# Performance work log

Measured on AMD Instinct MI355X. Metric: run time of the kernel, lower is better.

## Reference

```python
import jax, jax.numpy as jnp
import numpy as np

H = 4096; NH = 32; HD = 128; SCALE = HD ** -0.5
PREFILLS = [1024, 512, 768, 256]; DOFF = sum(PREFILLS)
DEC = 32; LMAX = 512; T = DOFF + DEC
NLORA = 4; RANK = 16
SEG = [0, 648, 1296, 1944, 2592]  # static lora segment offsets (cumsum of lens)
NEG = -1e30


def _rope_tables(pos):
    # pos: int array [...]; returns cos/sin of shape [..., HD]
    inv = 1.0 / (10000.0 ** (jnp.arange(0, HD, 2, dtype=jnp.float32) / HD))
    freqs = pos.astype(jnp.float32)[..., None] * inv
    emb = jnp.concatenate([freqs, freqs], axis=-1)
    return jnp.cos(emb), jnp.sin(emb)


def _apply_rope(x, cos, sin):
    # x: [..., HD]; cos/sin broadcastable to x
    x1, x2 = x[..., :HD // 2], x[..., HD // 2:]
    return x * cos + jnp.concatenate([-x2, x1], axis=-1) * sin


def _add_lora(y, x, wa, wb):
    # Punica add_lora: per-segment y += (x @ wa[i]) @ wb[i], segments static
    for i in range(NLORA):
        s, e = SEG[i], SEG[i + 1]
        y = y.at[s:e].add((x[s:e] @ wa[i]) @ wb[i])
    return y


def setup_inputs() -> dict:
    key = jax.random.key(0)
    ks = jax.random.split(key, 16)
    sc = np.float32(1.0 / np.sqrt(H))
    lsc = np.float32(1.0 / np.sqrt(H))
    inp = {
        "hidden_states": jax.random.normal(ks[0], (T, H), jnp.float32),
        "wq": jax.random.normal(ks[1], (H, H), jnp.float32) * sc,
        "wk": jax.random.normal(ks[2], (H, H), jnp.float32) * sc,
        "wv": jax.random.normal(ks[3], (H, H), jnp.float32) * sc,
        "wo": jax.random.normal(ks[4], (H, H), jnp.float32) * sc,
        "la_q": jax.random.normal(ks[5], (NLORA, H, RANK), jnp.float32) * lsc,
        "lb_q": jax.random.normal(ks[6], (NLORA, RANK, H), jnp.float32) * lsc,
        "la_k": jax.random.normal(ks[7], (NLORA, H, RANK), jnp.float32) * lsc,
        "lb_k": jax.random.normal(ks[8], (NLORA, RANK, H), jnp.float32) * lsc,
        "la_v": jax.random.normal(ks[9], (NLORA, H, RANK), jnp.float32) * lsc,
        "lb_v": jax.random.normal(ks[10], (NLORA, RANK, H), jnp.float32) * lsc,
        "la_o": jax.random.normal(ks[11], (NLORA, H, RANK), jnp.float32) * lsc,
        "lb_o": jax.random.normal(ks[12], (NLORA, RANK, H), jnp.float32) * lsc,
        "k_cache": jax.random.normal(ks[13], (DEC, LMAX, NH, HD), jnp.float32),
        "v_cache": jax.random.normal(ks[14], (DEC, LMAX, NH, HD), jnp.float32),
        "kv_lens": jax.random.randint(ks[15], (DEC,), 0, 450, jnp.int32),
    }
    return inp


def reference(hidden_states, wq, wk, wv, wo, la_q, lb_q, la_k, lb_k,
              la_v, lb_v, la_o, lb_o, k_cache, v_cache, kv_lens):
    # fused QKV + segmented batched LoRA
    q = _add_lora(hidden_states @ wq, hidden_states, la_q, lb_q)
    k = _add_lora(hidden_states @ wk, hidden_states, la_k, lb_k)
    v = _add_lora(hidden_states @ wv, hidden_states, la_v, lb_v)

    outs = []
    # ragged prefill: per-request causal attention with inline rotary (beg=0)
    off = 0
    for s_len in PREFILLS:
        qi = q[off:off + s_len].reshape(s_len, NH, HD)
        ki = k[off:off + s_len].reshape(s_len, NH, HD)
        vi = v[off:off + s_len].reshape(s_len, NH, HD)
        cos, sin = _rope_tables(jnp.arange(s_len))
        cos, sin = cos[:, None, :], sin[:, None, :]
        qi = _apply_rope(qi, cos, sin)
        ki = _apply_rope(ki, cos, sin)
        scores = jnp.einsum('qhd,khd->hqk', qi, ki) * SCALE
        causal = jnp.tril(jnp.ones((s_len, s_len), bool))
        scores = jnp.where(causal[None], scores, NEG)
        p = jax.nn.softmax(scores, axis=-1)
        outs.append(jnp.einsum('hqk,khd->qhd', p, vi).reshape(s_len, H))
        off += s_len

    # paged/batched decode: append new k/v at kv_lens, rope-on-the-fly attention
    qd = q[DOFF:].reshape(DEC, NH, HD)
    kd = k[DOFF:].reshape(DEC, NH, HD)
    vd = v[DOFF:].reshape(DEC, NH, HD)
    b = jnp.arange(DEC)
    kc = k_cache.at[b, kv_lens].set(kd)
    vc = v_cache.at[b, kv_lens].set(vd)
    cosq, sinq = _rope_tables(kv_lens)            # new token position = kv_len
    qd = _apply_rope(qd, cosq[:, None, :], sinq[:, None, :])
    cosk, sink = _rope_tables(jnp.arange(LMAX))   # cache positions 0..LMAX-1
    kc_r = _apply_rope(kc, cosk[None, :, None, :], sink[None, :, None, :])
    scores = jnp.einsum('bhd,blhd->bhl', qd, kc_r) * SCALE
    valid = jnp.arange(LMAX)[None, :] <= kv_lens[:, None]  # [DEC, LMAX]
    scores = jnp.where(valid[:, None, :], scores, NEG)
    p = jax.nn.softmax(scores, axis=-1)
    outs.append(jnp.einsum('bhl,blhd->bhd', p, vc).reshape(DEC, H))

    attn = jnp.concatenate(outs, axis=0)          # [T, H]
    o = attn @ wo
    o = _add_lora(o, attn, la_o, lb_o)
    return o
```

## Files before the change

kernel.cpp:

```cpp
#include <hip/hip_runtime.h>
#include <hip/hip_bf16.h>


#define H_    4096
#define NH_   32
#define HD_   128
#define T_    2592
#define DOFF_ 2560
#define DEC_  32
#define LMAX_ 512
#define RANK_ 16
#define MPAD_ 2816

__constant__ float SCALE_ = 0.08838834764831845f;

typedef __bf16 bf16x8 __attribute__((ext_vector_type(8)));
typedef __bf16 bf16x4 __attribute__((ext_vector_type(4)));
typedef float  f32x4  __attribute__((ext_vector_type(4)));

__device__ __forceinline__ void async_cp16(const __bf16* g, __bf16* l) {
    __builtin_amdgcn_global_load_lds(
        (const __attribute__((address_space(1))) void*)g,
        (__attribute__((address_space(3))) void*)l, 16, 0, 0);
}

__global__ __launch_bounds__(256)
void convert_bf16_kernel(const float* __restrict__ src, __bf16* __restrict__ dst, int n8)
{
    const int stride = gridDim.x * blockDim.x;
    for (int i = blockIdx.x * blockDim.x + threadIdx.x; i < n8; i += stride) {
        float4 a = ((const float4*)src)[i * 2];
        float4 b = ((const float4*)src)[i * 2 + 1];
        bf16x8 w;
        w[0] = (__bf16)a.x; w[1] = (__bf16)a.y; w[2] = (__bf16)a.z; w[3] = (__bf16)a.w;
        w[4] = (__bf16)b.x; w[5] = (__bf16)b.y; w[6] = (__bf16)b.z; w[7] = (__bf16)b.w;
        ((bf16x8*)dst)[i] = w;
    }
}

__global__ __launch_bounds__(256)
void transpose_bf16_kernel(const float* __restrict__ W0, const float* __restrict__ W1,
                           const float* __restrict__ W2,
                           __bf16* __restrict__ T0, __bf16* __restrict__ T1, __bf16* __restrict__ T2)
{
    const float* W = (blockIdx.z == 0) ? W0 : (blockIdx.z == 1 ? W1 : W2);
    __bf16* To     = (blockIdx.z == 0) ? T0 : (blockIdx.z == 1 ? T1 : T2);
    __shared__ float s[32][33];
    const int bx = blockIdx.x * 32;
    const int by = blockIdx.y * 32;
    const int r  = threadIdx.x >> 3;
    const int c4 = (threadIdx.x & 7) * 4;
    float4 v = *(const float4*)&W[(size_t)(by + r) * H_ + bx + c4];
    s[r][c4] = v.x; s[r][c4 + 1] = v.y; s[r][c4 + 2] = v.z; s[r][c4 + 3] = v.w;
    __syncthreads();
    bf16x4 o;
    o[0] = (__bf16)s[c4 + 0][r]; o[1] = (__bf16)s[c4 + 1][r];
    o[2] = (__bf16)s[c4 + 2][r]; o[3] = (__bf16)s[c4 + 3][r];
    *(bf16x4*)&To[(size_t)(bx + r) * H_ + by + c4] = o;
}

__global__ __launch_bounds__(256)
void lora_tmp_kernel(const float* __restrict__ X,
                     const float* __restrict__ la0, const float* __restrict__ la1,
                     const float* __restrict__ la2, __bf16* __restrict__ TMP16)
{
    const int r = blockIdx.x;
    const int si = (r < 648) ? 0 : (r < 1296 ? 1 : (r < 1944 ? 2 : 3));
    const int c    = threadIdx.x & 15;
    const int part = threadIdx.x >> 4;
    const float* xr = X + (size_t)r * H_;
    const float* wa0 = la0 + (size_t)si * H_ * RANK_;
    const float* wa1 = la1 + (size_t)si * H_ * RANK_;
    const float* wa2 = la2 + (size_t)si * H_ * RANK_;
    float s0 = 0.f, s1 = 0.f, s2 = 0.f;
    const int h0 = part * 256;
    for (int h = h0; h < h0 + 256; ++h) {
        const float xv = xr[h];
        s0 += xv * wa0[(size_t)h * RANK_ + c];
        s1 += xv * wa1[(size_t)h * RANK_ + c];
        s2 += xv * wa2[(size_t)h * RANK_ + c];
    }
    __shared__ float red[3][16][17];
    red[0][part][c] = s0; red[1][part][c] = s1; red[2][part][c] = s2;
    __syncthreads();
    if (threadIdx.x < 192) {
        const int z = threadIdx.x >> 6, cc = threadIdx.x & 63;
        float t = 0.f;
        if ((cc >> 4) == si) {
            #pragma unroll
            for (int p = 0; p < 16; ++p) t += red[z][p][cc & 15];
        }
        TMP16[((size_t)z * MPAD_ + r) * 64 + cc] = (__bf16)t;
    }
}

__global__ __launch_bounds__(256)
void lora_tmp_bf16_kernel(const __bf16* __restrict__ X,
                          const float* __restrict__ la, __bf16* __restrict__ TMPo16)
{
    const int r = blockIdx.x;
    const int si = (r < 648) ? 0 : (r < 1296 ? 1 : (r < 1944 ? 2 : 3));
    const float* wa = la + (size_t)si * H_ * RANK_;
    const int c    = threadIdx.x & 15;
    const int part = threadIdx.x >> 4;
    const __bf16* xr = X + (size_t)r * H_;
    float s = 0.f;
    const int h0 = part * 256;
    for (int h = h0; h < h0 + 256; ++h) s += (float)xr[h] * wa[(size_t)h * RANK_ + c];
    __shared__ float red[16][17];
    red[part][c] = s;
    __syncthreads();
    if (threadIdx.x < 64) {
        const int cc = threadIdx.x;
        float t = 0.f;
        if ((cc >> 4) == si) {
            #pragma unroll
            for (int p = 0; p < 16; ++p) t += red[p][cc & 15];
        }
        TMPo16[(size_t)r * 64 + cc] = (__bf16)t;
    }
}

__global__ __launch_bounds__(256)
void wb_build_kernel(const float* __restrict__ lbq, const float* __restrict__ lbk,
                     const float* __restrict__ lbv, const float* __restrict__ lbo,
                     __bf16* __restrict__ WB16, __bf16* __restrict__ WBo16)
{
    const int z = blockIdx.x;
    const int n = blockIdx.y * 256 + threadIdx.x;
    const float* lb = (z == 0) ? lbq : (z == 1 ? lbk : (z == 2 ? lbv : lbo));
    __bf16* dst = (z < 3) ? WB16 + ((size_t)z * H_ + n) * 64 : WBo16 + (size_t)n * 64;
    __bf16 row[64];
    #pragma unroll
    for (int si = 0; si < 4; ++si)
        #pragma unroll
        for (int c = 0; c < 16; ++c)
            row[si * 16 + c] = (__bf16)lb[((size_t)si * 16 + c) * H_ + n];
    #pragma unroll
    for (int i = 0; i < 8; ++i) *(bf16x8*)&dst[i * 8] = *(const bf16x8*)&row[i * 8];
}

__global__ __launch_bounds__(512, 2)
void gemm_qkv(const __bf16* __restrict__ A, const __bf16* __restrict__ Bt,
              const __bf16* __restrict__ TMP16, const __bf16* __restrict__ WB16,
              __bf16* __restrict__ O0, __bf16* __restrict__ O1, __bf16* __restrict__ O2, int M)
{
    const int hw = blockIdx.y * 21 + blockIdx.x;
    const int work = (hw & 7) * 126 + (hw >> 3);
    const int bm0 = (work % 21) * 128;
    const int bn0 = (work / 21) * 256;

    __shared__ __align__(16) __bf16 Asl[3][128 * 64];
    __shared__ __align__(16) __bf16 Bsl[3][256 * 64];

    const int tid = threadIdx.x, lane = tid & 63, wid = tid >> 6;
    const int wr = wid >> 2, wc = wid & 3;
    const int fr = lane & 15, fq = lane >> 4;

    int arow[2], aoff[2], brow[4], boff[4];
    #pragma unroll
    for (int i = 0; i < 2; ++i) {
        const int ci = i * 512 + tid;
        arow[i] = ci >> 3;
        aoff[i] = ((ci & 7) ^ (arow[i] & 7)) * 8;
    }
    #pragma unroll
    for (int i = 0; i < 4; ++i) {
        const int ci = i * 512 + tid;
        brow[i] = ci >> 3;
        boff[i] = ((ci & 7) ^ (brow[i] & 7)) * 8;
    }
    const __bf16* Ab = A  + (size_t)bm0 * H_;
    const __bf16* Bb = Bt + (size_t)bn0 * H_;

    auto stageA = [&](int buf, int kt2) {
        const int kb = kt2 * 64;
        #pragma unroll
        for (int i = 0; i < 2; ++i)
            async_cp16(Ab + (size_t)arow[i] * H_ + kb + aoff[i],
                       &Asl[buf][(i * 512 + wid * 64) * 8]);
    };
    auto stageB1 = [&](int buf, int kt2) {
        async_cp16(Bb + (size_t)brow[0] * H_ + kt2 * 64 + boff[0],
                   &Bsl[buf][(wid * 64) * 8]);
    };
    auto stageB3 = [&](int buf, int kt2) {
        const int kb = kt2 * 64;
        #pragma unroll
        for (int i = 1; i < 4; ++i)
            async_cp16(Bb + (size_t)brow[i] * H_ + kb + boff[i],
                       &Bsl[buf][(i * 512 + wid * 64) * 8]);
    };
    auto rdA = [&](int buf, int kh, int mi) -> bf16x8 {
        const int row = wr * 64 + mi * 16 + fr;
        const int pc  = (kh * 4 + fq) ^ (row & 7);
        return *(const bf16x8*)&Asl[buf][row * 64 + pc * 8];
    };
    auto rdB = [&](int buf, int kh, int nj) -> bf16x8 {
        const int row = wc * 64 + nj * 16 + fr;
        const int pc  = (kh * 4 + fq) ^ (row & 7);
        return *(const bf16x8*)&Bsl[buf][row * 64 + pc * 8];
    };

    f32x4 acc[4][4] = {};

    stageA(0, 0); stageB1(0, 0); stageB3(0, 0);
    stageA(1, 1); stageB1(1, 1); stageB3(1, 1);
    asm volatile("s_waitcnt vmcnt(6)");
    __builtin_amdgcn_sched_barrier(0);
    __builtin_amdgcn_s_barrier();

    const int NT = H_ / 64;
    int cur = 0, nxt = 2;
    for (int kt = 0; kt < NT; ++kt) {
        const bool pf = (kt + 2 < NT);
        bf16x8 af[4], bfr[4];

        #pragma unroll
        for (int mi = 0; mi < 4; ++mi) af[mi] = rdA(cur, 0, mi);
        #pragma unroll
        for (int nj = 0; nj < 4; ++nj) bfr[nj] = rdB(cur, 0, nj);
        if (pf) { stageA(nxt, kt + 2); stageB1(nxt, kt + 2); }
        __builtin_amdgcn_s_barrier();
        asm volatile("s_waitcnt lgkmcnt(0)");
        __builtin_amdgcn_sched_barrier(0);
        __builtin_amdgcn_s_setprio(1);
        #pragma unroll
        for (int mi = 0; mi < 4; ++mi)
            #pragma unroll
            for (int nj = 0; nj < 4; ++nj)
                acc[mi][nj] = __builtin_amdgcn_mfma_f32_16x16x32_bf16(af[mi], bfr[nj], acc[mi][nj], 0, 0, 0);
        __builtin_amdgcn_s_setprio(0);
        __builtin_amdgcn_s_barrier();

        #pragma unroll
        for (int mi = 0; mi < 4; ++mi) af[mi] = rdA(cur, 1, mi);
        #pragma unroll
        for (int nj = 0; nj < 4; ++nj) bfr[nj] = rdB(cur, 1, nj);
        if (pf) stageB3(nxt, kt + 2);
        __builtin_amdgcn_s_barrier();
        asm volatile("s_waitcnt lgkmcnt(0)");
        __builtin_amdgcn_sched_barrier(0);
        __builtin_amdgcn_s_setprio(1);
        #pragma unroll
        for (int mi = 0; mi < 4; ++mi)
            #pragma unroll
            for (int nj = 0; nj < 4; ++nj)
                acc[mi][nj] = __builtin_amdgcn_mfma_f32_16x16x32_bf16(af[mi], bfr[nj], acc[mi][nj], 0, 0, 0);
        __builtin_amdgcn_s_setprio(0);
        if (pf)               asm volatile("s_waitcnt vmcnt(6)");
        else if (kt + 1 < NT) asm volatile("s_waitcnt vmcnt(0)");
        __builtin_amdgcn_sched_barrier(0);
        __builtin_amdgcn_s_barrier();

        cur = (cur == 2) ? 0 : cur + 1;
        nxt = (nxt == 2) ? 0 : nxt + 1;
    }

    const int colbase = bn0 + wc * 64;
    const int mat = colbase >> 12;
    __bf16* O = (mat == 0) ? O0 : (mat == 1 ? O1 : O2);
    const __bf16* TPm = TMP16 + (size_t)mat * MPAD_ * 64;
    bf16x8 aT[4][2], bW[4][2];
    #pragma unroll
    for (int mi = 0; mi < 4; ++mi)
        #pragma unroll
        for (int kh = 0; kh < 2; ++kh)
            aT[mi][kh] = *(const bf16x8*)&TPm[(size_t)(bm0 + wr * 64 + mi * 16 + fr) * 64 + kh * 32 + fq * 8];
    #pragma unroll
    for (int nj = 0; nj < 4; ++nj)
        #pragma unroll
        for (int kh = 0; kh < 2; ++kh)
            bW[nj][kh] = *(const bf16x8*)&WB16[(size_t)(colbase + nj * 16 + fr) * 64 + kh * 32 + fq * 8];
    #pragma unroll
    for (int mi = 0; mi < 4; ++mi)
        #pragma unroll
        for (int nj = 0; nj < 4; ++nj) {
            acc[mi][nj] = __builtin_amdgcn_mfma_f32_16x16x32_bf16(aT[mi][0], bW[nj][0], acc[mi][nj], 0, 0, 0);
            acc[mi][nj] = __builtin_amdgcn_mfma_f32_16x16x32_bf16(aT[mi][1], bW[nj][1], acc[mi][nj], 0, 0, 0);
        }
    #pragma unroll
    for (int mi = 0; mi < 4; ++mi)
        #pragma unroll
        for (int nj = 0; nj < 4; ++nj) {
            const int cc = (colbase + nj * 16 + fr) & 4095;
            #pragma unroll
            for (int rr = 0; rr < 4; ++rr) {
                const int row = bm0 + wr * 64 + mi * 16 + fq * 4 + rr;
                if (row < M) O[(size_t)row * H_ + cc] = (__bf16)acc[mi][nj][rr];
            }
        }
}

__global__ __launch_bounds__(512, 2)
void gemm_out(const __bf16* __restrict__ A, const __bf16* __restrict__ Bt,
              const __bf16* __restrict__ TMPo16, const __bf16* __restrict__ WBo16,
              float* __restrict__ C, int M, int Ntot)
{
    const int NY = gridDim.y;
    const int total = gridDim.x * NY;
    const int bid = blockIdx.x * NY + blockIdx.y;
    const int q = total >> 3, r8 = total & 7;
    const int xcd = bid & 7, j = bid >> 3;
    const int swz = (xcd < r8 ? xcd * (q + 1) : r8 * (q + 1) + (xcd - r8) * q) + j;
    const int bm0 = (swz / NY) * 256;
    const int bn0 = (swz % NY) * 192;

    __shared__ __align__(16) __bf16 Asl[2][256 * 64];
    __shared__ __align__(16) __bf16 Bsl[2][192 * 64];

    const int tid = threadIdx.x, lane = tid & 63, wid = tid >> 6;
    const int wr = wid >> 2, wc = wid & 3;
    const int fr = lane & 15, fq = lane >> 4;

    int arow[4], aoff[4], brow[3], boff[3];
    #pragma unroll
    for (int i = 0; i < 4; ++i) {
        const int ci = i * 512 + tid;
        arow[i] = ci >> 3;
        aoff[i] = ((ci & 7) ^ (arow[i] & 7)) * 8;
    }
    #pragma unroll
    for (int i = 0; i < 3; ++i) {
        const int ci = i * 512 + tid;
        brow[i] = ci >> 3;
        boff[i] = ((ci & 7) ^ (brow[i] & 7)) * 8;
    }
    const __bf16* Ab = A  + (size_t)bm0 * H_;
    const __bf16* Bb = Bt + (size_t)bn0 * H_;

    auto stage = [&](int buf, int kt1) {
        const int kb = kt1 * 64;
        #pragma unroll
        for (int i = 0; i < 4; ++i)
            async_cp16(Ab + (size_t)arow[i] * H_ + kb + aoff[i],
                       &Asl[buf][(i * 512 + wid * 64) * 8]);
        #pragma unroll
        for (int i = 0; i < 3; ++i)
            async_cp16(Bb + (size_t)brow[i] * H_ + kb + boff[i],
                       &Bsl[buf][(i * 512 + wid * 64) * 8]);
    };
    auto rdA = [&](int buf, int kh, int mi) -> bf16x8 {
        const int row = wr * 128 + mi * 16 + fr;
        const int kc  = kh * 4 + fq;
        return *(const bf16x8*)&Asl[buf][row * 64 + ((kc ^ (row & 7)) << 3)];
    };
    auto rdB = [&](int buf, int kh, int nj) -> bf16x8 {
        const int row = wc * 48 + nj * 16 + fr;
        const int kc  = kh * 4 + fq;
        return *(const bf16x8*)&Bsl[buf][row * 64 + ((kc ^ (row & 7)) << 3)];
    };

    f32x4 acc[8][3] = {};

    stage(0, 0);
    asm volatile("s_waitcnt vmcnt(0)");
    __builtin_amdgcn_sched_barrier(0);
    __builtin_amdgcn_s_barrier();

    const int NT = H_ / 64;
    for (int kt = 0; kt < NT; ++kt) {
        const int cur = kt & 1, nb = cur ^ 1;
        const bool pf = (kt + 1 < NT);
        bf16x8 af[8], bfr[3];

        #pragma unroll
        for (int mi = 0; mi < 8; ++mi) af[mi] = rdA(cur, 0, mi);
        #pragma unroll
        for (int nj = 0; nj < 3; ++nj) bfr[nj] = rdB(cur, 0, nj);
        if (pf) stage(nb, kt + 1);
        __builtin_amdgcn_s_barrier();
        asm volatile("s_waitcnt lgkmcnt(0)");
        __builtin_amdgcn_sched_barrier(0);
        __builtin_amdgcn_s_setprio(1);
        #pragma unroll
        for (int mi = 0; mi < 8; ++mi)
            #pragma unroll
            for (int nj = 0; nj < 3; ++nj)
                acc[mi][nj] = __builtin_amdgcn_mfma_f32_16x16x32_bf16(af[mi], bfr[nj], acc[mi][nj], 0, 0, 0);
        __builtin_amdgcn_s_setprio(0);
        __builtin_amdgcn_s_barrier();

        #pragma unroll
        for (int mi = 0; mi < 8; ++mi) af[mi] = rdA(cur, 1, mi);
        #pragma unroll
        for (int nj = 0; nj < 3; ++nj) bfr[nj] = rdB(cur, 1, nj);
        __builtin_amdgcn_s_barrier();
        asm volatile("s_waitcnt lgkmcnt(0)");
        __builtin_amdgcn_sched_barrier(0);
        __builtin_amdgcn_s_setprio(1);
        #pragma unroll
        for (int mi = 0; mi < 8; ++mi)
            #pragma unroll
            for (int nj = 0; nj < 3; ++nj)
                acc[mi][nj] = __builtin_amdgcn_mfma_f32_16x16x32_bf16(af[mi], bfr[nj], acc[mi][nj], 0, 0, 0);
        __builtin_amdgcn_s_setprio(0);
        asm volatile("s_waitcnt vmcnt(0)");
        __builtin_amdgcn_sched_barrier(0);
        __builtin_amdgcn_s_barrier();
    }

    const int colw = bn0 + wc * 48;
    bf16x8 aT[8][2], bW[3][2];
    #pragma unroll
    for (int mi = 0; mi < 8; ++mi)
        #pragma unroll
        for (int kh = 0; kh < 2; ++kh)
            aT[mi][kh] = *(const bf16x8*)&TMPo16[(size_t)(bm0 + wr * 128 + mi * 16 + fr) * 64 + kh * 32 + fq * 8];
    #pragma unroll
    for (int nj = 0; nj < 3; ++nj)
        #pragma unroll
        for (int kh = 0; kh < 2; ++kh)
            bW[nj][kh] = *(const bf16x8*)&WBo16[(size_t)(colw + nj * 16 + fr) * 64 + kh * 32 + fq * 8];
    #pragma unroll
    for (int mi = 0; mi < 8; ++mi)
        #pragma unroll
        for (int nj = 0; nj < 3; ++nj) {
            acc[mi][nj] = __builtin_amdgcn_mfma_f32_16x16x32_bf16(aT[mi][0], bW[nj][0], acc[mi][nj], 0, 0, 0);
            acc[mi][nj] = __builtin_amdgcn_mfma_f32_16x16x32_bf16(aT[mi][1], bW[nj][1], acc[mi][nj], 0, 0, 0);
        }
    #pragma unroll
    for (int mi = 0; mi < 8; ++mi)
        #pragma unroll
        for (int nj = 0; nj < 3; ++nj) {
            const int col = colw + nj * 16 + fr;
            if (col < Ntot) {
                #pragma unroll
                for (int rr = 0; rr < 4; ++rr) {
                    const int row = bm0 + wr * 128 + mi * 16 + fq * 4 + rr;
                    if (row < M) C[(size_t)row * H_ + col] = acc[mi][nj][rr];
                }
            }
        }
}

__global__ void rope_table_kernel(float* __restrict__ cost, float* __restrict__ sint)
{
    const int p = blockIdx.x;
    const int i = threadIdx.x;
    const float inv = powf(10000.f, -(float)(2 * i) / (float)HD_);
    const float a = (float)p * inv;
    cost[p * 64 + i] = cosf(a);
    sint[p * 64 + i] = sinf(a);
}

__global__ __launch_bounds__(256)
void rope16_kernel(__bf16* __restrict__ q16, __bf16* __restrict__ k16,
                   const int* __restrict__ kv_lens,
                   const float* __restrict__ cost, const float* __restrict__ sint)
{
    const int r = blockIdx.x;
    int pos; bool dok;
    if (r < DOFF_) {
        if      (r < 1024) pos = r;
        else if (r < 1536) pos = r - 1024;
        else if (r < 2304) pos = r - 1536;
        else               pos = r - 2304;
        dok = true;
    } else {
        pos = kv_lens[r - DOFF_];
        dok = false;
    }
    const int tid = threadIdx.x;
    const int h = tid >> 3, sub = tid & 7;
    const int i0 = sub * 8;
    const size_t b1 = (size_t)r * H_ + h * HD_ + i0;
    const size_t b2 = b1 + 64;

    float cs[8], sn[8];
    #pragma unroll
    for (int j = 0; j < 8; ++j) { cs[j] = cost[pos * 64 + i0 + j]; sn[j] = sint[pos * 64 + i0 + j]; }

    {
        bf16x8 x1 = *(const bf16x8*)&q16[b1], x2 = *(const bf16x8*)&q16[b2];
        bf16x8 o1, o2;
        #pragma unroll
        for (int j = 0; j < 8; ++j) {
            const float f1 = (float)x1[j], f2 = (float)x2[j];
            o1[j] = (__bf16)(f1 * cs[j] - f2 * sn[j]);
            o2[j] = (__bf16)(f2 * cs[j] + f1 * sn[j]);
        }
        *(bf16x8*)&q16[b1] = o1; *(bf16x8*)&q16[b2] = o2;
    }
    if (dok) {
        bf16x8 x1 = *(const bf16x8*)&k16[b1], x2 = *(const bf16x8*)&k16[b2];
        bf16x8 o1, o2;
        #pragma unroll
        for (int j = 0; j < 8; ++j) {
            const float f1 = (float)x1[j], f2 = (float)x2[j];
            o1[j] = (__bf16)(f1 * cs[j] - f2 * sn[j]);
            o2[j] = (__bf16)(f2 * cs[j] + f1 * sn[j]);
        }
        *(bf16x8*)&k16[b1] = o1; *(bf16x8*)&k16[b2] = o2;
    }
}

__global__ __launch_bounds__(256)
void transpose_v_kernel(const __bf16* __restrict__ v16, __bf16* __restrict__ vT)
{
    __shared__ __bf16 s[64][136];
    const int tb = blockIdx.x;
    const int h  = blockIdx.y;
    const int tid = threadIdx.x;
    #pragma unroll
    for (int i = 0; i < 4; ++i) {
        const int idx = i * 256 + tid;
        const int row = idx >> 4;
        const int c8  = (idx & 15) * 8;
        *(bf16x8*)&s[row][c8] = *(const bf16x8*)&v16[(size_t)(tb * 64 + row) * H_ + h * HD_ + c8];
    }
    __syncthreads();
    #pragma unroll
    for (int i = 0; i < 4; ++i) {
        const int idx = i * 256 + tid;
        const int d = idx >> 3;
        const int c = idx & 7;
        bf16x8 w;
        #pragma unroll
        for (int j = 0; j < 8; ++j) w[j] = s[c * 8 + j][d];
        *(bf16x8*)&vT[(size_t)(h * HD_ + d) * T_ + tb * 64 + c * 8] = w;
    }
}

__global__ __launch_bounds__(256)
void prefill_attn_mfma(const __bf16* __restrict__ q16, const __bf16* __restrict__ k16,
                       const __bf16* __restrict__ vT, __bf16* __restrict__ attn16)
{
    const int qb = blockIdx.x;
    int soff, qoff;
    if      (qb < 16) { soff = 0;    qoff = qb * 64; }
    else if (qb < 24) { soff = 1024; qoff = (qb - 16) * 64; }
    else if (qb < 36) { soff = 1536; qoff = (qb - 24) * 64; }
    else              { soff = 2304; qoff = (qb - 36) * 64; }
    const int h = blockIdx.y;

    __shared__ __align__(16) __bf16 Kl[64 * 128];
    __shared__ __align__(16) __bf16 Vl[128 * 64];
    __shared__ __align__(16) __bf16 Pl[4][16 * 64];

    const int tid = threadIdx.x, lane = tid & 63, wid = tid >> 6;
    const int fr = lane & 15, fq = lane >> 4;

    const int grow0 = soff + qoff + wid * 16;
    bf16x8 qf[4];
    #pragma unroll
    for (int ks = 0; ks < 4; ++ks)
        qf[ks] = *(const bf16x8*)&q16[(size_t)(grow0 + fr) * H_ + h * HD_ + ks * 32 + fq * 8];

    float m[4], l[4];
    #pragma unroll
    for (int r = 0; r < 4; ++r) { m[r] = -1e30f; l[r] = 0.f; }
    f32x4 o[8] = {};

    const int ntiles = qoff / 64 + 1;
    for (int t = 0; t < ntiles; ++t) {
        const int kt = t * 64;
        #pragma unroll
        for (int i = 0; i < 4; ++i) {
            const int chunk = i * 256 + tid;
            const int row = chunk >> 4, c = chunk & 15;
            async_cp16(k16 + (size_t)(soff + kt + row) * H_ + h * HD_ + ((c ^ (row & 7)) * 8),
                       Kl + (size_t)(i * 256 + wid * 64) * 8);
        }
        #pragma unroll
        for (int i = 0; i < 4; ++i) {
            const int chunk = i * 256 + tid;
            const int row = chunk >> 3, c = chunk & 7;
            async_cp16(vT + (size_t)(h * HD_ + row) * T_ + soff + kt + ((c ^ (row & 7)) * 8),
                       Vl + (size_t)(i * 256 + wid * 64) * 8);
        }
        __syncthreads();

        f32x4 s[4] = {};
        #pragma unroll
        for (int sub = 0; sub < 4; ++sub)
            #pragma unroll
            for (int ks = 0; ks < 4; ++ks) {
                bf16x8 b = *(const bf16x8*)&Kl[(sub * 16 + fr) * 128 + (((ks * 4 + fq) ^ (fr & 7)) * 8)];
                s[sub] = __builtin_amdgcn_mfma_f32_16x16x32_bf16(qf[ks], b, s[sub], 0, 0, 0);
            }

        float p[4][4];
        #pragma unroll
        for (int sub = 0; sub < 4; ++sub)
            #pragma unroll
            for (int r = 0; r < 4; ++r) {
                const int qpos = qoff + wid * 16 + fq * 4 + r;
                const int kpos = kt + sub * 16 + fr;
                p[sub][r] = (kpos <= qpos) ? s[sub][r] * SCALE_ : -1e30f;
            }
        float fsc[4];
        #pragma unroll
        for (int r = 0; r < 4; ++r) {
            float tm = fmaxf(fmaxf(p[0][r], p[1][r]), fmaxf(p[2][r], p[3][r]));
            tm = fmaxf(tm, __shfl_xor(tm, 1));
            tm = fmaxf(tm, __shfl_xor(tm, 2));
            tm = fmaxf(tm, __shfl_xor(tm, 4));
            tm = fmaxf(tm, __shfl_xor(tm, 8));
            const float mn = fmaxf(m[r], tm);
            fsc[r] = __expf(m[r] - mn);
            m[r] = mn;
            float ls = 0.f;
            #pragma unroll
            for (int sub = 0; sub < 4; ++sub) {
                p[sub][r] = __expf(p[sub][r] - mn);
                ls += p[sub][r];
            }
            l[r] = l[r] * fsc[r] + ls;
        }
        #pragma unroll
        for (int c = 0; c < 8; ++c)
            #pragma unroll
            for (int r = 0; r < 4; ++r) o[c][r] *= fsc[r];

        #pragma unroll
        for (int sub = 0; sub < 4; ++sub)
            #pragma unroll
            for (int r = 0; r < 4; ++r) {
                const int qr = fq * 4 + r;
                Pl[wid][qr * 64 + ((sub * 16 + fr) ^ ((qr & 7) << 3))] = (__bf16)p[sub][r];
            }
        bf16x8 pa[2];
        #pragma unroll
        for (int a = 0; a < 2; ++a)
            pa[a] = *(const bf16x8*)&Pl[wid][fr * 64 + (((a * 4 + fq) ^ (fr & 7)) * 8)];

        #pragma unroll
        for (int a = 0; a < 2; ++a)
            #pragma unroll
            for (int c = 0; c < 8; ++c) {
                bf16x8 bv = *(const bf16x8*)&Vl[(c * 16 + fr) * 64 + (((a * 4 + fq) ^ (fr & 7)) * 8)];
                o[c] = __builtin_amdgcn_mfma_f32_16x16x32_bf16(pa[a], bv, o[c], 0, 0, 0);
            }
        __syncthreads();
    }

    float inv[4];
    #pragma unroll
    for (int r = 0; r < 4; ++r) {
        float ls = l[r];
        ls += __shfl_xor(ls, 1); ls += __shfl_xor(ls, 2);
        ls += __shfl_xor(ls, 4); ls += __shfl_xor(ls, 8);
        inv[r] = 1.f / ls;
    }
    #pragma unroll
    for (int c = 0; c < 8; ++c)
        #pragma unroll
        for (int r = 0; r < 4; ++r)
            attn16[(size_t)(grow0 + fq * 4 + r) * H_ + h * HD_ + c * 16 + fr] = (__bf16)(o[c][r] * inv[r]);
}

__global__ __launch_bounds__(256)
void decode_attn_kernel(const __bf16* __restrict__ q16, const __bf16* __restrict__ k16,
                        const __bf16* __restrict__ v16, const float* __restrict__ kc,
                        const float* __restrict__ vc, const int* __restrict__ kv_lens,
                        const float* __restrict__ cost, const float* __restrict__ sint,
                        __bf16* __restrict__ attn16)
{
    const int b = blockIdx.x, h = blockIdx.y;
    const int kvlen = kv_lens[b];
    const int L = kvlen + 1;
    const int tid = threadIdx.x, lane = tid & 63, w = tid >> 6;

    __shared__ float sc_s[LMAX_];
    __shared__ float red[4];
    __shared__ float oacc[HD_];

    const __bf16* qrow = q16 + (size_t)(DOFF_ + b) * H_ + h * HD_;
    const float q1 = (float)qrow[lane], q2 = (float)qrow[lane + 64];
    const __bf16* kdrow = k16 + (size_t)(DOFF_ + b) * H_ + h * HD_;

    for (int l = w; l < L; l += 4) {
        float k1, k2;
        if (l == kvlen) { k1 = (float)kdrow[lane]; k2 = (float)kdrow[lane + 64]; }
        else {
            const float* src = kc + (((size_t)b * LMAX_ + l) * NH_ + h) * HD_;
            k1 = src[lane]; k2 = src[lane + 64];
        }
        const float c = cost[l * 64 + lane], s = sint[l * 64 + lane];
        float d = q1 * (k1 * c - k2 * s) + q2 * (k2 * c + k1 * s);
        #pragma unroll
        for (int off = 1; off < 64; off <<= 1) d += __shfl_xor(d, off);
        if (lane == 0) sc_s[l] = d * SCALE_;
    }
    __syncthreads();

    float mx = -1e30f;
    for (int i = tid; i < L; i += 256) mx = fmaxf(mx, sc_s[i]);
    #pragma unroll
    for (int off = 1; off < 64; off <<= 1) mx = fmaxf(mx, __shfl_xor(mx, off));
    if (lane == 0) red[w] = mx;
    __syncthreads();
    mx = fmaxf(fmaxf(red[0], red[1]), fmaxf(red[2], red[3]));
    __syncthreads();

    float sum = 0.f;
    for (int i = tid; i < L; i += 256) { const float e = __expf(sc_s[i] - mx); sc_s[i] = e; sum += e; }
    #pragma unroll
    for (int off = 1; off < 64; off <<= 1) sum += __shfl_xor(sum, off);
    if (lane == 0) red[w] = sum;
    __syncthreads();
    sum = red[0] + red[1] + red[2] + red[3];
    const float inv = 1.f / sum;

    const int d = tid & 127, team = tid >> 7;
    const __bf16* vdrow = v16 + (size_t)(DOFF_ + b) * H_ + h * HD_;
    float acc = 0.f;
    for (int l = team; l < L; l += 2) {
        float vv;
        if (l == kvlen) vv = (float)vdrow[d];
        else            vv = vc[(((size_t)b * LMAX_ + l) * NH_ + h) * HD_ + d];
        acc += sc_s[l] * vv;
    }
    if (team == 1) oacc[d] = acc;
    __syncthreads();
    if (team == 0) attn16[(size_t)(DOFF_ + b) * H_ + h * HD_ + d] = (__bf16)((acc + oacc[d]) * inv);
}

extern "C" void kernel_launch(void* const* d_in, const int* in_sizes, int n_in,
                              void* d_out, int out_size, void* d_ws, size_t ws_size,
                              hipStream_t stream)
{
    const float* hs     = (const float*)d_in[0];
    const float* wq     = (const float*)d_in[1];
    const float* wk     = (const float*)d_in[2];
    const float* wv     = (const float*)d_in[3];
    const float* wo     = (const float*)d_in[4];
    const float* la_q   = (const float*)d_in[5];
    const float* lb_q   = (const float*)d_in[6];
    const float* la_k   = (const float*)d_in[7];
    const float* lb_k   = (const float*)d_in[8];
    const float* la_v   = (const float*)d_in[9];
    const float* lb_v   = (const float*)d_in[10];
    const float* la_o   = (const float*)d_in[11];
    const float* lb_o   = (const float*)d_in[12];
    const float* kcache = (const float*)d_in[13];
    const float* vcache = (const float*)d_in[14];
    const int*   kvlen  = (const int*)d_in[15];
    float* out = (float*)d_out;

    float*  costab = (float*)d_ws;
    float*  sintab = costab + 1024 * 64;
    __bf16* TMP16  = (__bf16*)(sintab + 1024 * 64);
    __bf16* TMPo16 = TMP16 + (size_t)3 * MPAD_ * 64;
    __bf16* WB16   = TMPo16 + (size_t)MPAD_ * 64;
    __bf16* WBo16  = WB16 + (size_t)3 * H_ * 64;
    __bf16* q16    = WBo16 + (size_t)4352 * 64;
    __bf16* k16    = q16 + (size_t)T_ * H_;
    __bf16* v16    = k16 + (size_t)T_ * H_;
    __bf16* hsb    = v16 + (size_t)T_ * H_;
    __bf16* wT     = hsb + (size_t)MPAD_ * H_;
    __bf16* vT     = wT + (size_t)H_ * H_;
    __bf16* attn16 = hsb;

    const int N8 = T_ * H_ / 8;

    rope_table_kernel<<<dim3(1024), dim3(64), 0, stream>>>(costab, sintab);
    convert_bf16_kernel<<<dim3(2048), dim3(256), 0, stream>>>(hs, hsb, N8);
    transpose_bf16_kernel<<<dim3(128, 128, 3), dim3(256), 0, stream>>>(
        wq, wk, wv, wT, wT + (size_t)H_ * H_, wT + (size_t)2 * H_ * H_);
    lora_tmp_kernel<<<dim3(T_), dim3(256), 0, stream>>>(hs, la_q, la_k, la_v, TMP16);
    wb_build_kernel<<<dim3(4, 16), dim3(256), 0, stream>>>(lb_q, lb_k, lb_v, lb_o, WB16, WBo16);
    gemm_qkv<<<dim3(21, 48), dim3(512), 0, stream>>>(
        hsb, wT, TMP16, WB16, q16, k16, v16, T_);
    rope16_kernel<<<dim3(T_), dim3(256), 0, stream>>>(q16, k16, kvlen, costab, sintab);
    transpose_v_kernel<<<dim3(40, 32), dim3(256), 0, stream>>>(v16, vT);
    prefill_attn_mfma<<<dim3(40, 32), dim3(256), 0, stream>>>(q16, k16, vT, attn16);
    decode_attn_kernel<<<dim3(DEC_, NH_), dim3(256), 0, stream>>>(q16, k16, v16, kcache, vcache,
                                                                  kvlen, costab, sintab, attn16);
    transpose_bf16_kernel<<<dim3(128, 128, 1), dim3(256), 0, stream>>>(wo, wo, wo, wT, wT, wT);
    lora_tmp_bf16_kernel<<<dim3(T_), dim3(256), 0, stream>>>(attn16, la_o, TMPo16);
    gemm_out<<<dim3(11, 22), dim3(512), 0, stream>>>(
        attn16, wT, TMPo16, WBo16, out, T_, H_);
}
```

Baseline: 971.5 us.

## Double-buffer prefill attention, lazy rescale, fuse hs convert with LoRA, bigger transpose tiles

Prefill attention now keeps two K/V LDS buffers and prefetches tile t+2 while computing tile t, using explicit vmcnt waits and raw barriers. It also skips the online-softmax rescale unless the running max grows by more than a threshold, and raises wave priority around the MFMA blocks. Separately, the hidden-state bf16 conversion is folded into the LoRA-A kernel, and the weight transpose moves to 64x64 tiles with 16-byte stores. The double buffering doubles LDS use, which may lower occupancy, and the lazy rescale relies on exp staying bounded when the max is stale.

After: 942.0 us. -3.0%, faster.

```diff
diff --git a/kernel.cpp b/kernel.cpp
--- a/kernel.cpp
+++ b/kernel.cpp
@@ -25,50 +25,24 @@
 }
 
 __global__ __launch_bounds__(256)
-void convert_bf16_kernel(const float* __restrict__ src, __bf16* __restrict__ dst, int n8)
-{
-    const int stride = gridDim.x * blockDim.x;
-    for (int i = blockIdx.x * blockDim.x + threadIdx.x; i < n8; i += stride) {
-        float4 a = ((const float4*)src)[i * 2];
-        float4 b = ((const float4*)src)[i * 2 + 1];
-        bf16x8 w;
-        w[0] = (__bf16)a.x; w[1] = (__bf16)a.y; w[2] = (__bf16)a.z; w[3] = (__bf16)a.w;
-        w[4] = (__bf16)b.x; w[5] = (__bf16)b.y; w[6] = (__bf16)b.z; w[7] = (__bf16)b.w;
-        ((bf16x8*)dst)[i] = w;
-    }
-}
-
-__global__ __launch_bounds__(256)
-void transpose_bf16_kernel(const float* __restrict__ W0, const float* __restrict__ W1,
-                           const float* __restrict__ W2,
-                           __bf16* __restrict__ T0, __bf16* __restrict__ T1, __bf16* __restrict__ T2)
-{
-    const float* W = (blockIdx.z == 0) ? W0 : (blockIdx.z == 1 ? W1 : W2);
-    __bf16* To     = (blockIdx.z == 0) ? T0 : (blockIdx.z == 1 ? T1 : T2);
-    __shared__ float s[32][33];
-    const int bx = blockIdx.x * 32;
-    const int by = blockIdx.y * 32;
-    const int r  = threadIdx.x >> 3;
-    const int c4 = (threadIdx.x & 7) * 4;
-    float4 v = *(const float4*)&W[(size_t)(by + r) * H_ + bx + c4];
-    s[r][c4] = v.x; s[r][c4 + 1] = v.y; s[r][c4 + 2] = v.z; s[r][c4 + 3] = v.w;
-    __syncthreads();
-    bf16x4 o;
-    o[0] = (__bf16)s[c4 + 0][r]; o[1] = (__bf16)s[c4 + 1][r];
-    o[2] = (__bf16)s[c4 + 2][r]; o[3] = (__bf16)s[c4 + 3][r];
-    *(bf16x4*)&To[(size_t)(bx + r) * H_ + by + c4] = o;
-}
-
-__global__ __launch_bounds__(256)
-void lora_tmp_kernel(const float* __restrict__ X,
-                     const float* __restrict__ la0, const float* __restrict__ la1,
-                     const float* __restrict__ la2, __bf16* __restrict__ TMP16)
+void hs_prep_kernel(const float* __restrict__ X, __bf16* __restrict__ Xb,
+                    const float* __restrict__ la0, const float* __restrict__ la1,
+                    const float* __restrict__ la2, __bf16* __restrict__ TMP16)
 {
     const int r = blockIdx.x;
+    const int tid = threadIdx.x;
+    const float* xr = X + (size_t)r * H_;
+    __bf16* br = Xb + (size_t)r * H_;
+    #pragma unroll
+    for (int i = 0; i < 4; ++i) {
+        float4 v = ((const float4*)xr)[tid + i * 256];
+        bf16x4 w; w[0] = (__bf16)v.x; w[1] = (__bf16)v.y; w[2] = (__bf16)v.z; w[3] = (__bf16)v.w;
+        ((bf16x4*)br)[tid + i * 256] = w;
+    }
+
     const int si = (r < 648) ? 0 : (r < 1296 ? 1 : (r < 1944 ? 2 : 3));
-    const int c    = threadIdx.x & 15;
-    const int part = threadIdx.x >> 4;
-    const float* xr = X + (size_t)r * H_;
+    const int c    = tid & 15;
+    const int part = tid >> 4;
     const float* wa0 = la0 + (size_t)si * H_ * RANK_;
     const float* wa1 = la1 + (size_t)si * H_ * RANK_;
     const float* wa2 = la2 + (size_t)si * H_ * RANK_;
@@ -83,14 +57,46 @@
     __shared__ float red[3][16][17];
     red[0][part][c] = s0; red[1][part][c] = s1; red[2][part][c] = s2;
     __syncthreads();
-    if (threadIdx.x < 192) {
-        const int z = threadIdx.x >> 6, cc = threadIdx.x & 63;
+    if (tid < 192) {
+        const int z = tid >> 6, cc = tid & 63;
         float t = 0.f;
         if ((cc >> 4) == si) {
             #pragma unroll
             for (int p = 0; p < 16; ++p) t += red[z][p][cc & 15];
         }
         TMP16[((size_t)z * MPAD_ + r) * 64 + cc] = (__bf16)t;
+    }
+}
+
+__global__ __launch_bounds__(256)
+void transpose_bf16_kernel(const float* __restrict__ W0, const float* __restrict__ W1,
+                           const float* __restrict__ W2,
+                           __bf16* __restrict__ T0, __bf16* __restrict__ T1, __bf16* __restrict__ T2)
+{
+    const float* W = (blockIdx.z == 0) ? W0 : (blockIdx.z == 1 ? W1 : W2);
+    __bf16* To     = (blockIdx.z == 0) ? T0 : (blockIdx.z == 1 ? T1 : T2);
+    __shared__ float s[64][65];
+    const int bx = blockIdx.x * 64;
+    const int by = blockIdx.y * 64;
+    const int tid = threadIdx.x;
+    #pragma unroll
+    for (int i = 0; i < 4; ++i) {
+        const int idx = i * 256 + tid;
+        const int r  = idx >> 4;
+        const int c4 = (idx & 15) * 4;
+        float4 v = *(const float4*)&W[(size_t)(by + r) * H_ + bx + c4];
+        s[r][c4] = v.x; s[r][c4 + 1] = v.y; s[r][c4 + 2] = v.z; s[r][c4 + 3] = v.w;
+    }
+    __syncthreads();
+    #pragma unroll
+    for (int i = 0; i < 2; ++i) {
+        const int idx = i * 256 + tid;
+        const int n  = idx >> 3;
+        const int kc = (idx & 7) * 8;
+        bf16x8 w;
+        #pragma unroll
+        for (int j = 0; j < 8; ++j) w[j] = (__bf16)s[kc + j][n];
+        *(bf16x8*)&To[(size_t)(bx + n) * H_ + by + kc] = w;
     }
 }
 
@@ -534,8 +540,8 @@
     else              { soff = 2304; qoff = (qb - 36) * 64; }
     const int h = blockIdx.y;
 
-    __shared__ __align__(16) __bf16 Kl[64 * 128];
-    __shared__ __align__(16) __bf16 Vl[128 * 64];
+    __shared__ __align__(16) __bf16 Kl[2][64 * 128];
+    __shared__ __align__(16) __bf16 Vl[2][128 * 64];
     __shared__ __align__(16) __bf16 Pl[4][16 * 64];
 
     const int tid = threadIdx.x, lane = tid & 63, wid = tid >> 6;
@@ -547,38 +553,57 @@
     for (int ks = 0; ks < 4; ++ks)
         qf[ks] = *(const bf16x8*)&q16[(size_t)(grow0 + fr) * H_ + h * HD_ + ks * 32 + fq * 8];
 
-    float m[4], l[4];
-    #pragma unroll
-    for (int r = 0; r < 4; ++r) { m[r] = -1e30f; l[r] = 0.f; }
-    f32x4 o[8] = {};
-
-    const int ntiles = qoff / 64 + 1;
-    for (int t = 0; t < ntiles; ++t) {
+    auto stageK = [&](int buf, int t) {
         const int kt = t * 64;
         #pragma unroll
         for (int i = 0; i < 4; ++i) {
             const int chunk = i * 256 + tid;
             const int row = chunk >> 4, c = chunk & 15;
             async_cp16(k16 + (size_t)(soff + kt + row) * H_ + h * HD_ + ((c ^ (row & 7)) * 8),
-                       Kl + (size_t)(i * 256 + wid * 64) * 8);
-        }
+                       Kl[buf] + (size_t)(i * 256 + wid * 64) * 8);
+        }
+    };
+    auto stageV = [&](int buf, int t) {
+        const int kt = t * 64;
         #pragma unroll
         for (int i = 0; i < 4; ++i) {
             const int chunk = i * 256 + tid;
             const int row = chunk >> 3, c = chunk & 7;
             async_cp16(vT + (size_t)(h * HD_ + row) * T_ + soff + kt + ((c ^ (row & 7)) * 8),
-                       Vl + (size_t)(i * 256 + wid * 64) * 8);
-        }
-        __syncthreads();
+                       Vl[buf] + (size_t)(i * 256 + wid * 64) * 8);
+        }
+    };
+
+    float m[4], l[4];
+    #pragma unroll
+    for (int r = 0; r < 4; ++r) { m[r] = -1e30f; l[r] = 0.f; }
+    f32x4 o[8] = {};
+
+    const int ntiles = qoff / 64 + 1;
+    stageK(0, 0); stageV(0, 0);
+    if (ntiles > 1) {
+        stageK(1, 1); stageV(1, 1);
+        asm volatile("s_waitcnt vmcnt(8)");
+    } else {
+        asm volatile("s_waitcnt vmcnt(0)");
+    }
+    __builtin_amdgcn_sched_barrier(0);
+    __builtin_amdgcn_s_barrier();
+
+    for (int t = 0; t < ntiles; ++t) {
+        const int b = t & 1;
+        const int kt = t * 64;
 
         f32x4 s[4] = {};
+        __builtin_amdgcn_s_setprio(1);
         #pragma unroll
         for (int sub = 0; sub < 4; ++sub)
             #pragma unroll
             for (int ks = 0; ks < 4; ++ks) {
-                bf16x8 b = *(const bf16x8*)&Kl[(sub * 16 + fr) * 128 + (((ks * 4 + fq) ^ (fr & 7)) * 8)];
-                s[sub] = __builtin_amdgcn_mfma_f32_16x16x32_bf16(qf[ks], b, s[sub], 0, 0, 0);
+                bf16x8 bk = *(const bf16x8*)&Kl[b][(sub * 16 + fr) * 128 + (((ks * 4 + fq) ^ (fr & 7)) * 8)];
+                s[sub] = __builtin_amdgcn_mfma_f32_16x16x32_bf16(qf[ks], bk, s[sub], 0, 0, 0);
             }
+        __builtin_amdgcn_s_setprio(0);
 
         float p[4][4];
         #pragma unroll
@@ -589,7 +614,7 @@
                 const int kpos = kt + sub * 16 + fr;
                 p[sub][r] = (kpos <= qpos) ? s[sub][r] * SCALE_ : -1e30f;
             }
-        float fsc[4];
+        float tm2[4];
         #pragma unroll
         for (int r = 0; r < 4; ++r) {
             float tm = fmaxf(fmaxf(p[0][r], p[1][r]), fmaxf(p[2][r], p[3][r]));
@@ -597,21 +622,32 @@
             tm = fmaxf(tm, __shfl_xor(tm, 2));
             tm = fmaxf(tm, __shfl_xor(tm, 4));
             tm = fmaxf(tm, __shfl_xor(tm, 8));
-            const float mn = fmaxf(m[r], tm);
-            fsc[r] = __expf(m[r] - mn);
-            m[r] = mn;
+            tm2[r] = tm;
+        }
+        bool need = false;
+        #pragma unroll
+        for (int r = 0; r < 4; ++r) need |= (tm2[r] > m[r] + 8.f);
+        if (__any(need)) {
+            #pragma unroll
+            for (int r = 0; r < 4; ++r) {
+                const float mn = fmaxf(m[r], tm2[r]);
+                const float f  = __expf(m[r] - mn);
+                m[r] = mn;
+                l[r] *= f;
+                #pragma unroll
+                for (int c = 0; c < 8; ++c) o[c][r] *= f;
+            }
+        }
+        #pragma unroll
+        for (int r = 0; r < 4; ++r) {
             float ls = 0.f;
             #pragma unroll
             for (int sub = 0; sub < 4; ++sub) {
-                p[sub][r] = __expf(p[sub][r] - mn);
+                p[sub][r] = __expf(p[sub][r] - m[r]);
                 ls += p[sub][r];
             }
-            l[r] = l[r] * fsc[r] + ls;
-        }
-        #pragma unroll
-        for (int c = 0; c < 8; ++c)
-            #pragma unroll
-            for (int r = 0; r < 4; ++r) o[c][r] *= fsc[r];
+            l[r] += ls;
+        }
 
         #pragma unroll
         for (int sub = 0; sub < 4; ++sub)
@@ -625,14 +661,25 @@
         for (int a = 0; a < 2; ++a)
             pa[a] = *(const bf16x8*)&Pl[wid][fr * 64 + (((a * 4 + fq) ^ (fr & 7)) * 8)];
 
+        __builtin_amdgcn_s_setprio(1);
         #pragma unroll
         for (int a = 0; a < 2; ++a)
             #pragma unroll
             for (int c = 0; c < 8; ++c) {
-                bf16x8 bv = *(const bf16x8*)&Vl[(c * 16 + fr) * 64 + (((a * 4 + fq) ^ (fr & 7)) * 8)];
+                bf16x8 bv = *(const bf16x8*)&Vl[b][(c * 16 + fr) * 64 + (((a * 4 + fq) ^ (fr & 7)) * 8)];
                 o[c] = __builtin_amdgcn_mfma_f32_16x16x32_bf16(pa[a], bv, o[c], 0, 0, 0);
             }
-        __syncthreads();
+        __builtin_amdgcn_s_setprio(0);
+
+        __builtin_amdgcn_s_barrier();
+        __builtin_amdgcn_sched_barrier(0);
+        if (t + 2 < ntiles) { stageK(b, t + 2); stageV(b, t + 2); }
+        if (t + 1 < ntiles) {
+            if (t + 2 < ntiles) asm volatile("s_waitcnt vmcnt(8)");
+            else                asm volatile("s_waitcnt vmcnt(0)");
+            __builtin_amdgcn_sched_barrier(0);
+            __builtin_amdgcn_s_barrier();
+        }
     }
 
     float inv[4];
@@ -753,13 +800,10 @@
     __bf16* vT     = wT + (size_t)H_ * H_;
     __bf16* attn16 = hsb;
 
-    const int N8 = T_ * H_ / 8;
-
     rope_table_kernel<<<dim3(1024), dim3(64), 0, stream>>>(costab, sintab);
-    convert_bf16_kernel<<<dim3(2048), dim3(256), 0, stream>>>(hs, hsb, N8);
-    transpose_bf16_kernel<<<dim3(128, 128, 3), dim3(256), 0, stream>>>(
+    hs_prep_kernel<<<dim3(T_), dim3(256), 0, stream>>>(hs, hsb, la_q, la_k, la_v, TMP16);
+    transpose_bf16_kernel<<<dim3(64, 64, 3), dim3(256), 0, stream>>>(
         wq, wk, wv, wT, wT + (size_t)H_ * H_, wT + (size_t)2 * H_ * H_);
-    lora_tmp_kernel<<<dim3(T_), dim3(256), 0, stream>>>(hs, la_q, la_k, la_v, TMP16);
     wb_build_kernel<<<dim3(4, 16), dim3(256), 0, stream>>>(lb_q, lb_k, lb_v, lb_o, WB16, WBo16);
     gemm_qkv<<<dim3(21, 48), dim3(512), 0, stream>>>(
         hsb, wT, TMP16, WB16, q16, k16, v16, T_);
@@ -768,7 +812,7 @@
     prefill_attn_mfma<<<dim3(40, 32), dim3(256), 0, stream>>>(q16, k16, vT, attn16);
     decode_attn_kernel<<<dim3(DEC_, NH_), dim3(256), 0, stream>>>(q16, k16, v16, kcache, vcache,
                                                                   kvlen, costab, sintab, attn16);
-    transpose_bf16_kernel<<<dim3(128, 128, 1), dim3(256), 0, stream>>>(wo, wo, wo, wT, wT, wT);
+    transpose_bf16_kernel<<<dim3(64, 64, 1), dim3(256), 0, stream>>>(wo, wo, wo, wT, wT, wT);
     lora_tmp_bf16_kernel<<<dim3(T_), dim3(256), 0, stream>>>(attn16, la_o, TMPo16);
     gemm_out<<<dim3(11, 22), dim3(512), 0, stream>>>(
         attn16, wT, TMPo16, WBo16, out, T_, H_);
```
